# Optimization experiments

Measured on AMD Instinct MI355X. Metric: run time of the kernel, lower is better.

The kernel has to match this reference:

```python
import jax, jax.numpy as jnp
import numpy as np

N_OSC = 60
B = 65536
DT = 0.1
STEPS = 10
PHI_INV = 2.0 / (1.0 + np.sqrt(5.0))


def setup_inputs() -> dict:
    key = jax.random.key(0)
    k1, k2, k3 = jax.random.split(key, 3)
    theta = jax.random.uniform(k1, (B, N_OSC), dtype=jnp.float32) * (2.0 * np.pi) - np.pi
    K = jax.random.normal(k2, (N_OSC, N_OSC), dtype=jnp.float32) * 0.1
    omega = jax.random.normal(k3, (N_OSC,), dtype=jnp.float32) * 0.1
    return {
        'theta': theta,
        'K': K,
        'omega': omega,
        'K_global': jnp.float32(PHI_INV),
        'coupling_mod': jnp.float32(0.6),        # phase_coupling['quasi_crystal']
        'neg_entropy_gate': jnp.float32(0.5),
        'critical_slow_factor': jnp.float32(0.1),
        'delta_s_neg': jnp.float32(0.8),          # NegativeEntropyState constant
        'relaxation_time': jnp.float32(5.0),      # NegativeEntropyState constant
    }


def reference(theta, K, omega, K_global, coupling_mod, neg_entropy_gate,
              critical_slow_factor, delta_s_neg, relaxation_time):
    n = theta.shape[-1]
    K_eff = K * coupling_mod                               # [n, n]
    critical_factor = 1.0 / (1.0 + critical_slow_factor * relaxation_time)
    eff_dt = DT * critical_factor
    boost = 1.0 + neg_entropy_gate * delta_s_neg
    scale = K_global * boost / n

    def step(th, _):
        # theta_diff[b, i, j] = th[b, j] - th[b, i]
        diff = th[..., None, :] - th[..., :, None]          # [B, n, n]
        coupling_sum = jnp.sum(K_eff * jnp.sin(diff), axis=-1)  # [B, n]
        th = th + eff_dt * (omega + scale * coupling_sum)
        th = jnp.arctan2(jnp.sin(th), jnp.cos(th))          # wrap to (-pi, pi]
        return th, None

    theta, _ = jax.lax.scan(step, theta, None, length=STEPS)
    cos_m = jnp.cos(theta).mean(axis=-1)
    sin_m = jnp.sin(theta).mean(axis=-1)
    coherence = jnp.sqrt(cos_m ** 2 + sin_m ** 2)           # [B]
    return theta, coherence
```

## Files before the change

### kernel.cpp

```cpp
#include <hip/hip_runtime.h>
#include <stdint.h>
#include <math.h>


#define B_TOTAL 65536
#define NOSC 60
#define STEPS 10

using short4v = __attribute__((ext_vector_type(4))) short;
using floatx4 = __attribute__((ext_vector_type(4))) float;

#if __has_builtin(__builtin_amdgcn_perm)
__device__ __forceinline__ unsigned int perm_b32(unsigned int s0, unsigned int s1, unsigned int sel) {
    return __builtin_amdgcn_perm(s0, s1, sel);
}
#else
__device__ __forceinline__ unsigned int perm_b32(unsigned int s0, unsigned int s1, unsigned int sel) {
    unsigned long long pool = ((unsigned long long)s0 << 32) | s1;
    unsigned int r = 0;
#pragma unroll
    for (int b = 0; b < 4; ++b) {
        unsigned int s = (sel >> (8 * b)) & 0xff;
        r |= ((unsigned int)((pool >> (8 * s)) & 0xff)) << (8 * b);
    }
    return r;
}
#endif

__device__ __forceinline__ unsigned int fbits(float x)        { return __builtin_bit_cast(unsigned int, x); }
__device__ __forceinline__ float        bitsf(unsigned int u) { return __builtin_bit_cast(float, u); }

#if __has_builtin(__builtin_amdgcn_mfma_f32_16x16x16bf16_1k)
__device__ __forceinline__ floatx4 mfma16(short4v a, short4v b, floatx4 c) {
    return __builtin_amdgcn_mfma_f32_16x16x16bf16_1k(a, b, c, 0, 0, 0);
}
#else
__device__ __forceinline__ floatx4 mfma16(short4v a, short4v b, floatx4 c) {
    asm("v_mfma_f32_16x16x16_bf16 %0, %1, %2, %0" : "+v"(c) : "v"(a), "v"(b));
    return c;
}
#endif

__device__ __forceinline__ unsigned int pack_hi_pair(float a, float b) {
    return perm_b32(fbits(b), fbits(a), 0x07060302u);
}

__global__ __launch_bounds__(64, 2)
void kuramoto_kernel(const float* __restrict__ theta_in,
                     const float* __restrict__ Kmat,
                     const float* __restrict__ omega,
                     const float* __restrict__ p_kglobal,
                     const float* __restrict__ p_cmod,
                     const float* __restrict__ p_gate,
                     const float* __restrict__ p_slow,
                     const float* __restrict__ p_dsneg,
                     const float* __restrict__ p_relax,
                     float* __restrict__ theta_out,
                     float* __restrict__ coh_out)
{
    const int lane = threadIdx.x & 63;
    const int lidx = lane & 15;
    const int quad = lane >> 4;

    const float kglobal = p_kglobal[0];
    const float cmod    = p_cmod[0];
    const float gate    = p_gate[0];
    const float slow    = p_slow[0];
    const float dsneg   = p_dsneg[0];
    const float relax   = p_relax[0];

    float eff_dt, scale;
    {
#pragma clang fp contract(off)
        const float a     = slow * relax;
        const float b     = 1.0f + a;
        const float crit  = 1.0f / b;
        eff_dt            = 0.1f * crit;
        const float boost = 1.0f + gate * dsneg;
        scale             = (kglobal * boost) / 60.0f;
    }

    const int batch0 = blockIdx.x * 16;
    const int brow   = (batch0 + lidx) * NOSC;

    short4v AH[4][4], AL[4][4];
#pragma unroll
    for (int nt = 0; nt < 4; ++nt) {
        const int i = nt * 16 + lidx;
        const bool okn = (i < NOSC);
#pragma unroll
        for (int kt = 0; kt < 4; ++kt) {
            const int k0 = kt * 16 + quad * 4;
            float kv[4];
            if (okn && (k0 + 3) < NOSC) {
                const float4 a = *(const float4*)(Kmat + i * NOSC + k0);
                kv[0] = a.x; kv[1] = a.y; kv[2] = a.z; kv[3] = a.w;
            } else {
#pragma unroll
                for (int j = 0; j < 4; ++j)
                    kv[j] = (okn && (k0 + j) < NOSC) ? Kmat[i * NOSC + k0 + j] : 0.0f;
            }
            short4v h, l;
#pragma unroll
            for (int j = 0; j < 4; ++j) {
                const float v = kv[j] * cmod;
                const unsigned int hb = fbits(v) & 0xffff0000u;
                const float rlo = v - bitsf(hb);
                h[j] = (short)(hb >> 16);
                l[j] = (short)(fbits(rlo) >> 16);
            }
            AH[nt][kt] = h;
            AL[nt][kt] = l;
        }
    }

    float th[4][4], sn[4][4], cn[4][4], omg[4][4];
#pragma unroll
    for (int nt = 0; nt < 4; ++nt) {
        const int o0 = nt * 16 + quad * 4;
        if (o0 + 3 < NOSC) {
            const float4 tv = *(const float4*)(theta_in + brow + o0);
            const float4 ov = *(const float4*)(omega + o0);
            th[nt][0] = tv.x; th[nt][1] = tv.y; th[nt][2] = tv.z; th[nt][3] = tv.w;
            omg[nt][0] = ov.x; omg[nt][1] = ov.y; omg[nt][2] = ov.z; omg[nt][3] = ov.w;
        } else {
#pragma unroll
            for (int r = 0; r < 4; ++r) { th[nt][r] = 0.0f; omg[nt][r] = 0.0f; }
        }
#pragma unroll
        for (int r = 0; r < 4; ++r)
            __sincosf(th[nt][r], &sn[nt][r], &cn[nt][r]);
    }

    const float PI_F = 3.14159274101257324f;
    const float C_HI = 6.28318548202514648f;
    const float C_LO = -1.7484556e-7f;

    for (int t = 0; t < STEPS; ++t) {
        floatx4 accS[4], accC[4];
#pragma unroll
        for (int nt = 0; nt < 4; ++nt) { accS[nt] = (floatx4)0.0f; accC[nt] = (floatx4)0.0f; }

#pragma unroll
        for (int kt = 0; kt < 4; ++kt) {
            union PU { unsigned int u[2]; short4v v; };
            PU bsh, bsl, bch, bcl;
            float sl[4], cl[4];
#pragma unroll
            for (int r = 0; r < 4; ++r) {
                const unsigned int us = fbits(sn[kt][r]);
                sl[r] = sn[kt][r] - bitsf(us & 0xffff0000u);
                const unsigned int uc = fbits(cn[kt][r]);
                cl[r] = cn[kt][r] - bitsf(uc & 0xffff0000u);
            }
            bsh.u[0] = pack_hi_pair(sn[kt][0], sn[kt][1]);
            bsh.u[1] = pack_hi_pair(sn[kt][2], sn[kt][3]);
            bsl.u[0] = pack_hi_pair(sl[0], sl[1]);
            bsl.u[1] = pack_hi_pair(sl[2], sl[3]);
            bch.u[0] = pack_hi_pair(cn[kt][0], cn[kt][1]);
            bch.u[1] = pack_hi_pair(cn[kt][2], cn[kt][3]);
            bcl.u[0] = pack_hi_pair(cl[0], cl[1]);
            bcl.u[1] = pack_hi_pair(cl[2], cl[3]);

#pragma unroll
            for (int nt = 0; nt < 4; ++nt) {
                accS[nt] = mfma16(AH[nt][kt], bsh.v, accS[nt]);
                accS[nt] = mfma16(AL[nt][kt], bsh.v, accS[nt]);
                accS[nt] = mfma16(AH[nt][kt], bsl.v, accS[nt]);
                accC[nt] = mfma16(AH[nt][kt], bch.v, accC[nt]);
                accC[nt] = mfma16(AL[nt][kt], bch.v, accC[nt]);
                accC[nt] = mfma16(AH[nt][kt], bcl.v, accC[nt]);
            }
        }

#pragma unroll
        for (int nt = 0; nt < 4; ++nt) {
#pragma unroll
            for (int r = 0; r < 4; ++r) {
                const float S = accS[nt][r];
                const float C = accC[nt][r];
                const float coup = cn[nt][r] * S - sn[nt][r] * C;
                float nth;
                {
#pragma clang fp contract(off)
                    const float t1 = scale * coup;
                    const float t2 = omg[nt][r] + t1;
                    const float t3 = eff_dt * t2;
                    nth = th[nt][r] + t3;
                }
                float n = 0.0f;
                n = (nth >=  PI_F) ?  1.0f : n;
                n = (nth <= -PI_F) ? -1.0f : n;
                float y = fmaf(n, -C_HI, nth);
                y = fmaf(n, -C_LO, y);
                th[nt][r] = y;
                __sincosf(y, &sn[nt][r], &cn[nt][r]);
            }
        }
    }

#pragma unroll
    for (int nt = 0; nt < 4; ++nt) {
        const int o0 = nt * 16 + quad * 4;
        if (o0 + 3 < NOSC) {
            float4 tv;
            tv.x = th[nt][0]; tv.y = th[nt][1]; tv.z = th[nt][2]; tv.w = th[nt][3];
            *(float4*)(theta_out + brow + o0) = tv;
        }
    }

    float pc = 0.0f, ps = 0.0f;
#pragma unroll
    for (int nt = 0; nt < 4; ++nt) {
        if (nt * 16 + quad * 4 < NOSC) {
#pragma unroll
            for (int r = 0; r < 4; ++r) { pc += cn[nt][r]; ps += sn[nt][r]; }
        }
    }
    pc += __shfl_xor(pc, 16);
    ps += __shfl_xor(ps, 16);
    pc += __shfl_xor(pc, 32);
    ps += __shfl_xor(ps, 32);
    if (quad == 0) {
        const float cm = pc / 60.0f;
        const float sm = ps / 60.0f;
        coh_out[batch0 + lidx] = sqrtf(cm * cm + sm * sm);
    }
}

extern "C" void kernel_launch(void* const* d_in, const int* in_sizes, int n_in,
                              void* d_out, int out_size, void* d_ws, size_t ws_size,
                              hipStream_t stream) {
    const float* theta = (const float*)d_in[0];
    const float* Kmat  = (const float*)d_in[1];
    const float* omg   = (const float*)d_in[2];
    const float* kg    = (const float*)d_in[3];
    const float* cmod  = (const float*)d_in[4];
    const float* gate  = (const float*)d_in[5];
    const float* slow  = (const float*)d_in[6];
    const float* dsn   = (const float*)d_in[7];
    const float* relax = (const float*)d_in[8];
    float* out = (float*)d_out;

    kuramoto_kernel<<<dim3(B_TOTAL / 16), dim3(64), 0, stream>>>(
        theta, Kmat, omg, kg, cmod, gate, slow, dsn, relax,
        out, out + (size_t)B_TOTAL * NOSC);
}
```

Baseline: 125.3 us.

## Switch coupling matmul to 32x32x16 bf16 MFMA tiles with 32 batches per wave

```diff
diff --git a/kernel.cpp b/kernel.cpp
--- a/kernel.cpp
+++ b/kernel.cpp
@@ -7,8 +7,9 @@
 #define NOSC 60
 #define STEPS 10
 
-using short4v = __attribute__((ext_vector_type(4))) short;
-using floatx4 = __attribute__((ext_vector_type(4))) float;
+using short8v  = __attribute__((ext_vector_type(8))) short;
+using floatx16 = __attribute__((ext_vector_type(16))) float;
+using bf16x8   = __attribute__((ext_vector_type(8))) __bf16;
 
 #if __has_builtin(__builtin_amdgcn_perm)
 __device__ __forceinline__ unsigned int perm_b32(unsigned int s0, unsigned int s1, unsigned int sel) {
@@ -30,22 +31,21 @@
 __device__ __forceinline__ unsigned int fbits(float x)        { return __builtin_bit_cast(unsigned int, x); }
 __device__ __forceinline__ float        bitsf(unsigned int u) { return __builtin_bit_cast(float, u); }
 
-#if __has_builtin(__builtin_amdgcn_mfma_f32_16x16x16bf16_1k)
-__device__ __forceinline__ floatx4 mfma16(short4v a, short4v b, floatx4 c) {
-    return __builtin_amdgcn_mfma_f32_16x16x16bf16_1k(a, b, c, 0, 0, 0);
-}
+__device__ __forceinline__ floatx16 mfma32(short8v a, short8v b, floatx16 c) {
+#if __has_builtin(__builtin_amdgcn_mfma_f32_32x32x16_bf16)
+    return __builtin_amdgcn_mfma_f32_32x32x16_bf16(
+        __builtin_bit_cast(bf16x8, a), __builtin_bit_cast(bf16x8, b), c, 0, 0, 0);
 #else
-__device__ __forceinline__ floatx4 mfma16(short4v a, short4v b, floatx4 c) {
-    asm("v_mfma_f32_16x16x16_bf16 %0, %1, %2, %0" : "+v"(c) : "v"(a), "v"(b));
+    asm("v_mfma_f32_32x32x16_bf16 %0, %1, %2, %0" : "+v"(c) : "v"(a), "v"(b));
     return c;
-}
 #endif
+}
 
 __device__ __forceinline__ unsigned int pack_hi_pair(float a, float b) {
     return perm_b32(fbits(b), fbits(a), 0x07060302u);
 }
 
-__global__ __launch_bounds__(64, 2)
+__global__ __launch_bounds__(64)
 void kuramoto_kernel(const float* __restrict__ theta_in,
                      const float* __restrict__ Kmat,
                      const float* __restrict__ omega,
@@ -59,8 +59,8 @@
                      float* __restrict__ coh_out)
 {
     const int lane = threadIdx.x & 63;
-    const int lidx = lane & 15;
-    const int quad = lane >> 4;
+    const int c    = lane & 31;
+    const int h    = lane >> 5;
 
     const float kglobal = p_kglobal[0];
     const float cmod    = p_cmod[0];
@@ -80,151 +80,167 @@
         scale             = (kglobal * boost) / 60.0f;
     }
 
-    const int batch0 = blockIdx.x * 16;
-    const int brow   = (batch0 + lidx) * NOSC;
-
-    short4v AH[4][4], AL[4][4];
-#pragma unroll
-    for (int nt = 0; nt < 4; ++nt) {
-        const int i = nt * 16 + lidx;
-        const bool okn = (i < NOSC);
-#pragma unroll
-        for (int kt = 0; kt < 4; ++kt) {
-            const int k0 = kt * 16 + quad * 4;
-            float kv[4];
-            if (okn && (k0 + 3) < NOSC) {
-                const float4 a = *(const float4*)(Kmat + i * NOSC + k0);
-                kv[0] = a.x; kv[1] = a.y; kv[2] = a.z; kv[3] = a.w;
+    const int batch0 = blockIdx.x * 32;
+    const int brow   = (batch0 + c) * NOSC;
+
+    short8v AH[2][4], AL[2][4];
+#pragma unroll
+    for (int ob = 0; ob < 2; ++ob) {
+        const int m = 32 * ob + c;
+        const bool okm = (m < NOSC);
+#pragma unroll
+        for (int kb = 0; kb < 4; ++kb) {
+            const int base = 16 * kb + 4 * h;
+            float kv[8];
+            if (okm && (base + 11) < NOSC) {
+                const float4 a = *(const float4*)(Kmat + m * NOSC + base);
+                const float4 b = *(const float4*)(Kmat + m * NOSC + base + 8);
+                kv[0]=a.x; kv[1]=a.y; kv[2]=a.z; kv[3]=a.w;
+                kv[4]=b.x; kv[5]=b.y; kv[6]=b.z; kv[7]=b.w;
             } else {
 #pragma unroll
-                for (int j = 0; j < 4; ++j)
-                    kv[j] = (okn && (k0 + j) < NOSC) ? Kmat[i * NOSC + k0 + j] : 0.0f;
-            }
-            short4v h, l;
-#pragma unroll
-            for (int j = 0; j < 4; ++j) {
+                for (int j = 0; j < 8; ++j) {
+                    const int col = base + (j & 3) + 8 * (j >> 2);
+                    kv[j] = (okm && col < NOSC) ? Kmat[m * NOSC + col] : 0.0f;
+                }
+            }
+            short8v hh, ll;
+#pragma unroll
+            for (int j = 0; j < 8; ++j) {
                 const float v = kv[j] * cmod;
                 const unsigned int hb = fbits(v) & 0xffff0000u;
                 const float rlo = v - bitsf(hb);
-                h[j] = (short)(hb >> 16);
-                l[j] = (short)(fbits(rlo) >> 16);
-            }
-            AH[nt][kt] = h;
-            AL[nt][kt] = l;
-        }
-    }
-
-    float th[4][4], sn[4][4], cn[4][4], omg[4][4];
-#pragma unroll
-    for (int nt = 0; nt < 4; ++nt) {
-        const int o0 = nt * 16 + quad * 4;
-        if (o0 + 3 < NOSC) {
-            const float4 tv = *(const float4*)(theta_in + brow + o0);
-            const float4 ov = *(const float4*)(omega + o0);
-            th[nt][0] = tv.x; th[nt][1] = tv.y; th[nt][2] = tv.z; th[nt][3] = tv.w;
-            omg[nt][0] = ov.x; omg[nt][1] = ov.y; omg[nt][2] = ov.z; omg[nt][3] = ov.w;
-        } else {
-#pragma unroll
-            for (int r = 0; r < 4; ++r) { th[nt][r] = 0.0f; omg[nt][r] = 0.0f; }
-        }
-#pragma unroll
-        for (int r = 0; r < 4; ++r)
-            __sincosf(th[nt][r], &sn[nt][r], &cn[nt][r]);
+                hh[j] = (short)(hb >> 16);
+                ll[j] = (short)(fbits(rlo) >> 16);
+            }
+            AH[ob][kb] = hh;
+            AL[ob][kb] = ll;
+        }
+    }
+
+    float th[2][16], sn[2][16], cn[2][16], omg[2][16];
+#pragma unroll
+    for (int ob = 0; ob < 2; ++ob) {
+#pragma unroll
+        for (int g = 0; g < 4; ++g) {
+            const int o0 = 32 * ob + 8 * g + 4 * h;
+            const int rb = 4 * g;
+            if (o0 + 3 < NOSC) {
+                const float4 tv = *(const float4*)(theta_in + brow + o0);
+                const float4 ov = *(const float4*)(omega + o0);
+                th[ob][rb+0] = tv.x; th[ob][rb+1] = tv.y; th[ob][rb+2] = tv.z; th[ob][rb+3] = tv.w;
+                omg[ob][rb+0] = ov.x; omg[ob][rb+1] = ov.y; omg[ob][rb+2] = ov.z; omg[ob][rb+3] = ov.w;
+            } else {
+#pragma unroll
+                for (int m = 0; m < 4; ++m) { th[ob][rb+m] = 0.0f; omg[ob][rb+m] = 0.0f; }
+            }
+#pragma unroll
+            for (int m = 0; m < 4; ++m)
+                __sincosf(th[ob][rb+m], &sn[ob][rb+m], &cn[ob][rb+m]);
+        }
     }
 
     const float PI_F = 3.14159274101257324f;
     const float C_HI = 6.28318548202514648f;
     const float C_LO = -1.7484556e-7f;
 
+#pragma unroll 1
     for (int t = 0; t < STEPS; ++t) {
-        floatx4 accS[4], accC[4];
-#pragma unroll
-        for (int nt = 0; nt < 4; ++nt) { accS[nt] = (floatx4)0.0f; accC[nt] = (floatx4)0.0f; }
-
-#pragma unroll
-        for (int kt = 0; kt < 4; ++kt) {
-            union PU { unsigned int u[2]; short4v v; };
-            PU bsh, bsl, bch, bcl;
-            float sl[4], cl[4];
-#pragma unroll
-            for (int r = 0; r < 4; ++r) {
-                const unsigned int us = fbits(sn[kt][r]);
-                sl[r] = sn[kt][r] - bitsf(us & 0xffff0000u);
-                const unsigned int uc = fbits(cn[kt][r]);
-                cl[r] = cn[kt][r] - bitsf(uc & 0xffff0000u);
-            }
-            bsh.u[0] = pack_hi_pair(sn[kt][0], sn[kt][1]);
-            bsh.u[1] = pack_hi_pair(sn[kt][2], sn[kt][3]);
-            bsl.u[0] = pack_hi_pair(sl[0], sl[1]);
-            bsl.u[1] = pack_hi_pair(sl[2], sl[3]);
-            bch.u[0] = pack_hi_pair(cn[kt][0], cn[kt][1]);
-            bch.u[1] = pack_hi_pair(cn[kt][2], cn[kt][3]);
-            bcl.u[0] = pack_hi_pair(cl[0], cl[1]);
-            bcl.u[1] = pack_hi_pair(cl[2], cl[3]);
-
-#pragma unroll
-            for (int nt = 0; nt < 4; ++nt) {
-                accS[nt] = mfma16(AH[nt][kt], bsh.v, accS[nt]);
-                accS[nt] = mfma16(AL[nt][kt], bsh.v, accS[nt]);
-                accS[nt] = mfma16(AH[nt][kt], bsl.v, accS[nt]);
-                accC[nt] = mfma16(AH[nt][kt], bch.v, accC[nt]);
-                accC[nt] = mfma16(AL[nt][kt], bch.v, accC[nt]);
-                accC[nt] = mfma16(AH[nt][kt], bcl.v, accC[nt]);
-            }
-        }
-
-#pragma unroll
-        for (int nt = 0; nt < 4; ++nt) {
-#pragma unroll
-            for (int r = 0; r < 4; ++r) {
-                const float S = accS[nt][r];
-                const float C = accC[nt][r];
-                const float coup = cn[nt][r] * S - sn[nt][r] * C;
+        floatx16 aS0, aS1, aC0, aC1;
+        const floatx16 Z = (floatx16)0.0f;
+
+#pragma unroll
+        for (int kb = 0; kb < 4; ++kb) {
+            const int obp = kb >> 1;
+            const int r0  = (kb & 1) * 8;
+
+            float sl_[8], cl_[8];
+#pragma unroll
+            for (int s = 0; s < 8; ++s) {
+                const unsigned us = fbits(sn[obp][r0+s]);
+                sl_[s] = sn[obp][r0+s] - bitsf(us & 0xffff0000u);
+                const unsigned uc = fbits(cn[obp][r0+s]);
+                cl_[s] = cn[obp][r0+s] - bitsf(uc & 0xffff0000u);
+            }
+            union BU { unsigned u[4]; short8v v; };
+            BU Bsh, Bsl, Bch, Bcl;
+#pragma unroll
+            for (int p = 0; p < 4; ++p) {
+                Bsh.u[p] = pack_hi_pair(sn[obp][r0+2*p], sn[obp][r0+2*p+1]);
+                Bsl.u[p] = pack_hi_pair(sl_[2*p], sl_[2*p+1]);
+                Bch.u[p] = pack_hi_pair(cn[obp][r0+2*p], cn[obp][r0+2*p+1]);
+                Bcl.u[p] = pack_hi_pair(cl_[2*p], cl_[2*p+1]);
+            }
+
+            aS0 = mfma32(AH[0][kb], Bsh.v, (kb == 0) ? Z : aS0);
+            aS1 = mfma32(AH[1][kb], Bsh.v, (kb == 0) ? Z : aS1);
+            aC0 = mfma32(AH[0][kb], Bch.v, (kb == 0) ? Z : aC0);
+            aC1 = mfma32(AH[1][kb], Bch.v, (kb == 0) ? Z : aC1);
+            aS0 = mfma32(AL[0][kb], Bsh.v, aS0);
+            aS1 = mfma32(AL[1][kb], Bsh.v, aS1);
+            aC0 = mfma32(AL[0][kb], Bch.v, aC0);
+            aC1 = mfma32(AL[1][kb], Bch.v, aC1);
+            aS0 = mfma32(AH[0][kb], Bsl.v, aS0);
+            aS1 = mfma32(AH[1][kb], Bsl.v, aS1);
+            aC0 = mfma32(AH[0][kb], Bcl.v, aC0);
+            aC1 = mfma32(AH[1][kb], Bcl.v, aC1);
+        }
+
+#pragma unroll
+        for (int ob = 0; ob < 2; ++ob) {
+            const floatx16 &aS = ob ? aS1 : aS0;
+            const floatx16 &aC = ob ? aC1 : aC0;
+#pragma unroll
+            for (int r = 0; r < 16; ++r) {
+                const float S = aS[r];
+                const float C = aC[r];
+                const float coup = cn[ob][r] * S - sn[ob][r] * C;
                 float nth;
                 {
 #pragma clang fp contract(off)
                     const float t1 = scale * coup;
-                    const float t2 = omg[nt][r] + t1;
+                    const float t2 = omg[ob][r] + t1;
                     const float t3 = eff_dt * t2;
-                    nth = th[nt][r] + t3;
+                    nth = th[ob][r] + t3;
                 }
                 float n = 0.0f;
                 n = (nth >=  PI_F) ?  1.0f : n;
                 n = (nth <= -PI_F) ? -1.0f : n;
                 float y = fmaf(n, -C_HI, nth);
                 y = fmaf(n, -C_LO, y);
-                th[nt][r] = y;
-                __sincosf(y, &sn[nt][r], &cn[nt][r]);
-            }
-        }
-    }
-
-#pragma unroll
-    for (int nt = 0; nt < 4; ++nt) {
-        const int o0 = nt * 16 + quad * 4;
-        if (o0 + 3 < NOSC) {
-            float4 tv;
-            tv.x = th[nt][0]; tv.y = th[nt][1]; tv.z = th[nt][2]; tv.w = th[nt][3];
-            *(float4*)(theta_out + brow + o0) = tv;
+                th[ob][r] = y;
+                __sincosf(y, &sn[ob][r], &cn[ob][r]);
+            }
+        }
+    }
+
+#pragma unroll
+    for (int ob = 0; ob < 2; ++ob) {
+#pragma unroll
+        for (int g = 0; g < 4; ++g) {
+            const int o0 = 32 * ob + 8 * g + 4 * h;
+            const int rb = 4 * g;
+            if (o0 + 3 < NOSC) {
+                float4 tv;
+                tv.x = th[ob][rb+0]; tv.y = th[ob][rb+1];
+                tv.z = th[ob][rb+2]; tv.w = th[ob][rb+3];
+                *(float4*)(theta_out + brow + o0) = tv;
+            }
         }
     }
 
     float pc = 0.0f, ps = 0.0f;
 #pragma unroll
-    for (int nt = 0; nt < 4; ++nt) {
-        if (nt * 16 + quad * 4 < NOSC) {
-#pragma unroll
-            for (int r = 0; r < 4; ++r) { pc += cn[nt][r]; ps += sn[nt][r]; }
-        }
-    }
-    pc += __shfl_xor(pc, 16);
-    ps += __shfl_xor(ps, 16);
+    for (int ob = 0; ob < 2; ++ob)
+#pragma unroll
+        for (int r = 0; r < 16; ++r) { pc += cn[ob][r]; ps += sn[ob][r]; }
+    pc -= h ? 4.0f : 0.0f;
     pc += __shfl_xor(pc, 32);
     ps += __shfl_xor(ps, 32);
-    if (quad == 0) {
+    if (h == 0) {
         const float cm = pc / 60.0f;
         const float sm = ps / 60.0f;
-        coh_out[batch0 + lidx] = sqrtf(cm * cm + sm * sm);
+        coh_out[batch0 + c] = sqrtf(cm * cm + sm * sm);
     }
 }
 
@@ -242,7 +258,7 @@
     const float* relax = (const float*)d_in[8];
     float* out = (float*)d_out;
 
-    kuramoto_kernel<<<dim3(B_TOTAL / 16), dim3(64), 0, stream>>>(
+    kuramoto_kernel<<<dim3(B_TOTAL / 32), dim3(64), 0, stream>>>(
         theta, Kmat, omg, kg, cmod, gate, slow, dsn, relax,
         out, out + (size_t)B_TOTAL * NOSC);
 }
```

New measurement: 120.0 us. 4.3% less time.
